# Kernel optimization log

Hardware: AMD Instinct MI355X
Metric: run time of the kernel (lower is better)

## Reference

```python
import jax, jax.numpy as jnp
import numpy as np

N_HEAD = 16
W = 128  # one-sided window = attention_window // 2


def setup_inputs() -> dict:
    key = jax.random.key(0)
    ks = jax.random.split(key, 6)
    B, S, D = 4, 1536, 1024
    init = lambda k: jax.random.normal(k, (D, D), jnp.float32) * 0.02
    return {
        "x": jax.random.normal(ks[0], (B, S, D), jnp.float32),
        "Wq": init(ks[1]), "bq": jnp.zeros((D,), jnp.float32),
        "Wk": init(ks[2]),
        "Wv": init(ks[3]), "bv": jnp.zeros((D,), jnp.float32),
        "Wo": init(ks[4]), "bo": jnp.zeros((D,), jnp.float32),
    }


def _local_attention(q, k, v, w):
    """Sliding-window attention. q,k,v: [B,H,S,Dh]; q,k pre-scaled.
    Returns context [B,H,S,Dh] and banded logits qk [B,S,H,2w+1] (fp32)."""
    B, H, S, Dh = q.shape
    C = S // w  # number of w-sized query chunks
    pad = [(0, 0), (0, 0), (w, w), (0, 0)]
    kp = jnp.pad(k, pad)
    vp = jnp.pad(v, pad)
    # key/value chunks: chunk c sees padded positions [c*w, c*w + 3w)
    idx = jnp.arange(C)[:, None] * w + jnp.arange(3 * w)[None, :]  # [C,3w]
    kc = kp[:, :, idx]                      # [B,H,C,3w,Dh]
    vc = vp[:, :, idx]                      # [B,H,C,3w,Dh]
    qc = q.reshape(B, H, C, w, Dh)          # [B,H,C,w,Dh]
    scores = jnp.einsum('bhcxd,bhcyd->bhcxy', qc, kc)  # [B,H,C,w,3w]
    # extract diagonal band: query x attends to chunk-local keys y = x .. x+2w
    xi = jnp.arange(w)[:, None]             # [w,1]
    jj = jnp.arange(2 * w + 1)[None, :]     # [1,2w+1]
    y = xi + jj                             # [w,2w+1], values in [0,3w)
    band = jnp.take_along_axis(scores, y[None, None, None], axis=-1)  # [B,H,C,w,2w+1]
    # mask positions whose absolute key index falls outside [0,S)
    key_pos = jnp.arange(C)[:, None, None] * w + xi[None] + jj[None] - w  # [C,w,2w+1]
    valid = (key_pos >= 0) & (key_pos < S)
    band = jnp.where(valid[None, None], band, -jnp.inf)
    prob = jax.nn.softmax(band.astype(jnp.float32), axis=-1).astype(q.dtype)
    # scatter band probs back to chunk layout, then contract with value chunks
    scat = jnp.zeros_like(scores).at[..., xi, y].set(prob)  # [B,H,C,w,3w]
    ctx = jnp.einsum('bhcxy,bhcyd->bhcxd', scat, vc).reshape(B, H, S, Dh)
    qk = band.astype(jnp.float32).reshape(B, H, S, 2 * w + 1).transpose(0, 2, 1, 3)
    return ctx, qk


def reference(x, Wq, bq, Wk, Wv, bv, Wo, bo):
    B, S, D = x.shape
    H, Dh = N_HEAD, D // N_HEAD
    scale = Dh ** (-0.25)
    q = ((x @ Wq.T + bq).reshape(B, S, H, Dh).transpose(0, 2, 1, 3)) * scale
    k = ((x @ Wk.T).reshape(B, S, H, Dh).transpose(0, 2, 1, 3)) * scale
    v = (x @ Wv.T + bv).reshape(B, S, H, Dh).transpose(0, 2, 1, 3)
    ctx, qk = _local_attention(q, k, v, W)
    wv = ctx.transpose(0, 2, 1, 3).reshape(B, S, D)
    out = wv @ Wo.T + bo
    return out, qk
```

## Files before the change

### kernel.cpp

```cpp
#include <hip/hip_runtime.h>

#define S_LEN  1536
#define NH     16
#define DHEAD  64
#define WIN    128
#define BAND   257
#define DMODEL 1024
#define BATCH  4
#define MROWS  (BATCH * S_LEN)

#define SQ    32
#define SWIN  (SQ + 2*WIN)
#define WKEYS 320
#define PST   296

#define NEG_BIG (-3.0e38f)

typedef __attribute__((ext_vector_type(8))) short frag_ab;
typedef __attribute__((ext_vector_type(4))) float frag_cd;
typedef __attribute__((ext_vector_type(8))) unsigned short ushort8v;

__device__ __forceinline__ unsigned short f2bf(float f) {
  unsigned u = __float_as_uint(f);
  u += 0x7FFFu + ((u >> 16) & 1u);
  return (unsigned short)(u >> 16);
}
__device__ __forceinline__ float bf2f(unsigned short h) {
  return __uint_as_float(((unsigned)h) << 16);
}

__device__ __forceinline__ void gload16(const unsigned short* g, unsigned short* l) {
  __builtin_amdgcn_global_load_lds(
      (const __attribute__((address_space(1))) unsigned int*)g,
      (__attribute__((address_space(3))) unsigned int*)l, 16, 0, 0);
}

__device__ __forceinline__ int swz4(int r) { return (r & 3) ^ ((r >> 2) & 3); }

__global__ __launch_bounds__(256)
void convert_hilo(const float* __restrict__ src, unsigned short* __restrict__ hi,
                  unsigned short* __restrict__ lo, int n4)
{
  const int i = blockIdx.x * 256 + threadIdx.x;
  if (i >= n4) return;
  const float4 v = reinterpret_cast<const float4*>(src)[i];
  unsigned short h0 = f2bf(v.x), h1 = f2bf(v.y), h2 = f2bf(v.z), h3 = f2bf(v.w);
  unsigned short l0 = f2bf(v.x - bf2f(h0)), l1 = f2bf(v.y - bf2f(h1));
  unsigned short l2 = f2bf(v.z - bf2f(h2)), l3 = f2bf(v.w - bf2f(h3));
  uint2 hp, lp;
  hp.x = (unsigned)h0 | ((unsigned)h1 << 16); hp.y = (unsigned)h2 | ((unsigned)h3 << 16);
  lp.x = (unsigned)l0 | ((unsigned)l1 << 16); lp.y = (unsigned)l2 | ((unsigned)l3 << 16);
  reinterpret_cast<uint2*>(hi)[i] = hp;
  reinterpret_cast<uint2*>(lo)[i] = lp;
}

__global__ __launch_bounds__(256)
void mfma_gemm_qkv(const unsigned short* __restrict__ Ah_g,
                   const unsigned short* __restrict__ Al_g,
                   const unsigned short* __restrict__ Bh_g,
                   const unsigned short* __restrict__ Bl_g,
                   const float* __restrict__ bq, const float* __restrict__ bv,
                   float scale,
                   unsigned short* __restrict__ Qh, unsigned short* __restrict__ Ql,
                   unsigned short* __restrict__ Kh, unsigned short* __restrict__ Kl,
                   unsigned short* __restrict__ Vh, unsigned short* __restrict__ Vl)
{
  __shared__ __align__(16) unsigned short Ah[256*32];
  __shared__ __align__(16) unsigned short Al[256*32];
  __shared__ __align__(16) unsigned short Bh[128*32];
  __shared__ __align__(16) unsigned short Bl[128*32];

  const int t    = threadIdx.x;
  const int wave = t >> 6, lane = t & 63;
  const int wr   = wave >> 1, wc = wave & 1;

  const int bid  = blockIdx.x;
  const int xcd  = bid & 7;
  const int r    = bid >> 3;
  const int n0   = (xcd*3 + (r % 3)) * 128;
  const int m0   = (r / 3) * 256;

  frag_cd acc[8][4];
#pragma unroll
  for (int i = 0; i < 8; ++i)
#pragma unroll
    for (int j = 0; j < 4; ++j) acc[i][j] = (frag_cd){0.f,0.f,0.f,0.f};

  const int srow = lane >> 2;
  const int scol = ((lane & 3) ^ swz4(srow)) * 8;
  const unsigned short* aSh = Ah_g + (size_t)(m0 + wave*64 + srow) * DMODEL + scol;
  const unsigned short* aSl = Al_g + (size_t)(m0 + wave*64 + srow) * DMODEL + scol;
  const unsigned short* bSh = Bh_g + (size_t)(n0 + wave*32 + srow) * DMODEL + scol;
  const unsigned short* bSl = Bl_g + (size_t)(n0 + wave*32 + srow) * DMODEL + scol;
  unsigned short* aDh = &Ah[(wave*64)*32];
  unsigned short* aDl = &Al[(wave*64)*32];
  unsigned short* bDh = &Bh[(wave*32)*32];
  unsigned short* bDl = &Bl[(wave*32)*32];

  const int l16  = lane & 15;
  const int koff = ((lane >> 4) * 8) ^ (swz4(l16) * 8);
  int ofsA[8], ofsB[4];
#pragma unroll
  for (int i = 0; i < 8; ++i) ofsA[i] = (wr*128 + i*16 + l16)*32 + koff;
#pragma unroll
  for (int j = 0; j < 4; ++j) ofsB[j] = (wc*64 + j*16 + l16)*32 + koff;

  for (int k0 = 0; k0 < DMODEL; k0 += 32) {
#pragma unroll
    for (int u = 0; u < 4; ++u) {
      gload16(aSh + (size_t)u*16*DMODEL + k0, aDh + u*16*32);
      gload16(aSl + (size_t)u*16*DMODEL + k0, aDl + u*16*32);
    }
#pragma unroll
    for (int u = 0; u < 2; ++u) {
      gload16(bSh + (size_t)u*16*DMODEL + k0, bDh + u*16*32);
      gload16(bSl + (size_t)u*16*DMODEL + k0, bDl + u*16*32);
    }
    __syncthreads();

    frag_ab bh[4], blr[4];
#pragma unroll
    for (int j = 0; j < 4; ++j) {
      bh[j]  = *reinterpret_cast<const frag_ab*>(&Bh[ofsB[j]]);
      blr[j] = *reinterpret_cast<const frag_ab*>(&Bl[ofsB[j]]);
    }
#pragma unroll
    for (int i = 0; i < 8; ++i) {
      frag_ab ah  = *reinterpret_cast<const frag_ab*>(&Ah[ofsA[i]]);
      frag_ab alr = *reinterpret_cast<const frag_ab*>(&Al[ofsA[i]]);
#pragma unroll
      for (int j = 0; j < 4; ++j) {
        acc[i][j] = __builtin_amdgcn_mfma_f32_16x16x32_bf16(ah,  bh[j],  acc[i][j], 0,0,0);
        acc[i][j] = __builtin_amdgcn_mfma_f32_16x16x32_bf16(ah,  blr[j], acc[i][j], 0,0,0);
        acc[i][j] = __builtin_amdgcn_mfma_f32_16x16x32_bf16(alr, bh[j],  acc[i][j], 0,0,0);
      }
    }
    __syncthreads();
  }

  const int rg = lane >> 4;
  const int which = n0 >> 10;
  const float sc = (which < 2) ? scale : 1.0f;
  const float* bias = (which == 0) ? bq : ((which == 2) ? bv : nullptr);
  unsigned short* Dh = (which == 0) ? Qh : ((which == 1) ? Kh : Vh);
  unsigned short* Dl = (which == 0) ? Ql : ((which == 1) ? Kl : Vl);
#pragma unroll
  for (int j = 0; j < 4; ++j) {
    const int n  = n0 + wc*64 + j*16 + l16;
    const int nn = n & 1023;
    const float bval = bias ? bias[nn] : 0.f;
    const int hh = nn >> 6, dh = nn & 63;
#pragma unroll
    for (int i = 0; i < 8; ++i) {
#pragma unroll
      for (int r2 = 0; r2 < 4; ++r2) {
        const int m = m0 + wr*128 + i*16 + rg*4 + r2;
        const int b = m / S_LEN;
        const int s = m - b * S_LEN;
        const size_t idx = ((size_t)((b*NH + hh)*S_LEN + s))*DHEAD + dh;
        const float v = (acc[i][j][r2] + bval) * sc;
        const unsigned short hv = f2bf(v);
        Dh[idx] = hv;
        Dl[idx] = f2bf(v - bf2f(hv));
      }
    }
  }
}

__global__ __launch_bounds__(256)
void mfma_gemm_wo(const unsigned short* __restrict__ Ah_g,
                  const unsigned short* __restrict__ Al_g,
                  const unsigned short* __restrict__ Bh_g,
                  const unsigned short* __restrict__ Bl_g,
                  const float* __restrict__ bias,
                  float* __restrict__ Cf)
{
  __shared__ __align__(16) unsigned short Ah[128*32];
  __shared__ __align__(16) unsigned short Al[128*32];
  __shared__ __align__(16) unsigned short Bh[64*32];
  __shared__ __align__(16) unsigned short Bl[64*32];

  const int t    = threadIdx.x;
  const int wave = t >> 6, lane = t & 63;
  const int wr   = wave >> 1, wc = wave & 1;
  const int m0   = blockIdx.y * 128;
  const int n0   = blockIdx.x * 64;

  frag_cd acc[4][2];
#pragma unroll
  for (int i = 0; i < 4; ++i)
#pragma unroll
    for (int j = 0; j < 2; ++j) acc[i][j] = (frag_cd){0.f,0.f,0.f,0.f};

  const int srow = lane >> 2;
  const int scol = ((lane & 3) ^ swz4(srow)) * 8;
  size_t rbase[2];
#pragma unroll
  for (int u = 0; u < 2; ++u) {
    const int m = m0 + wave*32 + u*16 + srow;
    const int b = m / S_LEN;
    const int s = m - b * S_LEN;
    rbase[u] = ((size_t)(b*NH))*S_LEN*DHEAD + (size_t)s*DHEAD;
  }
  const unsigned short* pb = Bh_g + (size_t)(n0 + wave*16 + srow) * DMODEL + scol;
  const unsigned short* qb = Bl_g + (size_t)(n0 + wave*16 + srow) * DMODEL + scol;
  unsigned short* lA0 = &Ah[(wave*32)*32];
  unsigned short* lA1 = &Ah[(wave*32+16)*32];
  unsigned short* lL0 = &Al[(wave*32)*32];
  unsigned short* lL1 = &Al[(wave*32+16)*32];
  unsigned short* lB  = &Bh[(wave*16)*32];
  unsigned short* lBl = &Bl[(wave*16)*32];

  const int l16  = lane & 15;
  const int koff = ((lane >> 4) * 8) ^ (swz4(l16) * 8);
  int ofsA[4], ofsB[2];
#pragma unroll
  for (int i = 0; i < 4; ++i) ofsA[i] = (wr*64 + i*16 + l16)*32 + koff;
#pragma unroll
  for (int j = 0; j < 2; ++j) ofsB[j] = (wc*32 + j*16 + l16)*32 + koff;

  for (int k0 = 0; k0 < DMODEL; k0 += 32) {
    const int kk = k0 + scol;
    const size_t aoff = ((size_t)(kk >> 6))*(S_LEN*DHEAD) + (kk & 63);
    gload16(Ah_g + rbase[0] + aoff, lA0);
    gload16(Ah_g + rbase[1] + aoff, lA1);
    gload16(Al_g + rbase[0] + aoff, lL0);
    gload16(Al_g + rbase[1] + aoff, lL1);
    gload16(pb, lB);  gload16(qb, lBl);
    pb += 32; qb += 32;
    __syncthreads();

    frag_ab ah[4], alr[4], bh[2], blr[2];
#pragma unroll
    for (int i = 0; i < 4; ++i) {
      ah[i]  = *reinterpret_cast<const frag_ab*>(&Ah[ofsA[i]]);
      alr[i] = *reinterpret_cast<const frag_ab*>(&Al[ofsA[i]]);
    }
#pragma unroll
    for (int j = 0; j < 2; ++j) {
      bh[j]  = *reinterpret_cast<const frag_ab*>(&Bh[ofsB[j]]);
      blr[j] = *reinterpret_cast<const frag_ab*>(&Bl[ofsB[j]]);
    }
#pragma unroll
    for (int i = 0; i < 4; ++i)
#pragma unroll
      for (int j = 0; j < 2; ++j) {
        acc[i][j] = __builtin_amdgcn_mfma_f32_16x16x32_bf16(ah[i],  bh[j],  acc[i][j], 0,0,0);
        acc[i][j] = __builtin_amdgcn_mfma_f32_16x16x32_bf16(ah[i],  blr[j], acc[i][j], 0,0,0);
        acc[i][j] = __builtin_amdgcn_mfma_f32_16x16x32_bf16(alr[i], bh[j],  acc[i][j], 0,0,0);
      }
    __syncthreads();
  }

  const int rg = lane >> 4;
#pragma unroll
  for (int j = 0; j < 2; ++j) {
    const int n = n0 + wc*32 + j*16 + l16;
    const float bval = bias[n];
#pragma unroll
    for (int i = 0; i < 4; ++i) {
#pragma unroll
      for (int r = 0; r < 4; ++r) {
        const int m = m0 + wr*64 + i*16 + rg*4 + r;
        Cf[(size_t)m * DMODEL + n] = acc[i][j][r] + bval;
      }
    }
  }
}

__global__ __launch_bounds__(256, 3)
void attn_fused(const unsigned short* __restrict__ Qh_g, const unsigned short* __restrict__ Ql_g,
                const unsigned short* __restrict__ Kh_g, const unsigned short* __restrict__ Kl_g,
                const unsigned short* __restrict__ Vh_g, const unsigned short* __restrict__ Vl_g,
                float* __restrict__ qk,
                unsigned short* __restrict__ ctx_hi, unsigned short* __restrict__ ctx_lo)
{
  __shared__ __align__(16) unsigned char arena[48384];
  unsigned short* Khs = (unsigned short*)(arena);
  unsigned short* Kls = (unsigned short*)(arena + 20480);
  unsigned short* Qhs = (unsigned short*)(arena + 40960);
  unsigned short* Qls = (unsigned short*)(arena + 43008);
  unsigned short* Pth = (unsigned short*)(arena);
  unsigned short* Ptl = (unsigned short*)(arena + 18944);
  float*          red = (float*)(arena + 37888);
  unsigned short* Vs  = (unsigned short*)(arena + 38912);

  const int t    = threadIdx.x;
  const int wave = t >> 6, lane = t & 63;

  const int lid  = blockIdx.x;
  const int xcd  = lid & 7;
  const int idx  = lid >> 3;
  const int qblk = xcd*6 + (idx % 6);
  const int hb   = idx / 6;
  const int h    = hb & 15, b = hb >> 4;
  const int qa0  = qblk * SQ;
  const int ws0  = qa0 - WIN;

  const size_t ho = (size_t)(b*NH + h) * S_LEN * DHEAD;
  const unsigned short* Qh = Qh_g + ho;
  const unsigned short* Ql = Ql_g + ho;
  const unsigned short* Kh = Kh_g + ho;
  const unsigned short* Kl = Kl_g + ho;
  const unsigned short* Vh = Vh_g + ho;
  const unsigned short* Vl = Vl_g + ho;

  const int l16  = lane & 15;
  const int grp  = lane >> 4;
  const int koff  = grp * 8;
  const int koffs = koff ^ (swz4(l16) * 8);
  const int srow = lane >> 2;
  const int scol = ((lane & 3) ^ swz4(srow)) * 8;

  frag_cd acc[2][5];
#pragma unroll
  for (int tm = 0; tm < 2; ++tm)
#pragma unroll
    for (int tn = 0; tn < 5; ++tn) acc[tm][tn] = (frag_cd){0.f,0.f,0.f,0.f};

  for (int p = 0; p < 2; ++p) {
    const int d0 = p * 32;
    if (p) __syncthreads();
#pragma unroll
    for (int i = 0; i < 5; ++i) {
      const int r0 = wave*80 + i*16;
      const ptrdiff_t g = (ptrdiff_t)(ws0 + r0 + srow) * DHEAD + d0 + scol;
      gload16(Kh + g, &Khs[r0*32]);
      gload16(Kl + g, &Kls[r0*32]);
    }
    if (wave < 2) {
      const unsigned short* src = wave ? Ql : Qh;
      unsigned short* dst = wave ? Qls : Qhs;
#pragma unroll
      for (int i = 0; i < 2; ++i) {
        const ptrdiff_t g = (ptrdiff_t)(qa0 + i*16 + srow) * DHEAD + d0 + scol;
        gload16(src + g, &dst[i*16*32]);
      }
    }
    __syncthreads();

    frag_ab ah[2], al[2];
#pragma unroll
    for (int tm = 0; tm < 2; ++tm) {
      const int o = (tm*16 + l16)*32 + koffs;
      ah[tm] = *reinterpret_cast<const frag_ab*>(&Qhs[o]);
      al[tm] = *reinterpret_cast<const frag_ab*>(&Qls[o]);
    }
#pragma unroll
    for (int tn = 0; tn < 5; ++tn) {
      const int o = (wave*80 + tn*16 + l16)*32 + koffs;
      frag_ab bh = *reinterpret_cast<const frag_ab*>(&Khs[o]);
      frag_ab bl = *reinterpret_cast<const frag_ab*>(&Kls[o]);
#pragma unroll
      for (int tm = 0; tm < 2; ++tm) {
        acc[tm][tn] = __builtin_amdgcn_mfma_f32_16x16x32_bf16(ah[tm], bh, acc[tm][tn], 0,0,0);
        acc[tm][tn] = __builtin_amdgcn_mfma_f32_16x16x32_bf16(ah[tm], bl, acc[tm][tn], 0,0,0);
        acc[tm][tn] = __builtin_amdgcn_mfma_f32_16x16x32_bf16(al[tm], bh, acc[tm][tn], 0,0,0);
      }
    }
  }

#pragma unroll
  for (int tm = 0; tm < 2; ++tm)
#pragma unroll
    for (int tn = 0; tn < 5; ++tn)
#pragma unroll
      for (int r = 0; r < 4; ++r) {
        const int x  = tm*16 + grp*4 + r;
        const int yw = wave*80 + tn*16 + l16;
        const int j  = yw - x;
        const int kp = ws0 + yw;
        const bool ok = (j >= 0) & (j < BAND) & (kp >= 0) & (kp < S_LEN);
        acc[tm][tn][r] = ok ? acc[tm][tn][r] : NEG_BIG;
      }
#pragma unroll
  for (int tm = 0; tm < 2; ++tm)
#pragma unroll
    for (int r = 0; r < 4; ++r) {
      const int x = tm*16 + grp*4 + r;
      float* qrow = qk + ((size_t)(b*S_LEN + qa0 + x)*NH + h) * BAND;
#pragma unroll
      for (int tn = 0; tn < 5; ++tn) {
        const int yw = wave*80 + tn*16 + l16;
        const int j  = yw - x;
        if (j >= 0 && j < BAND) qrow[j] = acc[tm][tn][r];
      }
    }

  __syncthreads();

  const unsigned short* vsrc = (wave == 3) ? Vl : Vh;
  const int vrow0 = (wave == 3) ? 8 : 0;
  ushort8v RA[5], RB[5];

  auto loadVto = [&](int c, ushort8v* R) {
    const int d0 = c*8;
#pragma unroll
    for (int it = 0; it < 5; ++it) {
      const int y = it*64 + lane;
      ushort8v v = {0,0,0,0,0,0,0,0};
      if (y < SWIN) {
        const int kp = ws0 + y;
        if (kp >= 0 && kp < S_LEN)
          v = *reinterpret_cast<const ushort8v*>(vsrc + (size_t)kp*DHEAD + d0);
      }
      R[it] = v;
    }
  };
  auto writeVfrom = [&](ushort8v* R) {
#pragma unroll
    for (int it = 0; it < 5; ++it) {
      const int y = it*64 + lane;
      if (y < SWIN) {
#pragma unroll
        for (int e = 0; e < 8; ++e) Vs[(vrow0 + e)*PST + y] = R[it][e];
      }
    }
  };

  if (wave >= 2) loadVto(0, RA);
#pragma unroll
  for (int tm = 0; tm < 2; ++tm)
#pragma unroll
    for (int r = 0; r < 4; ++r) {
      float m = acc[tm][0][r];
#pragma unroll
      for (int tn = 1; tn < 5; ++tn) m = fmaxf(m, acc[tm][tn][r]);
      m = fmaxf(m, __shfl_xor(m, 1, 64));
      m = fmaxf(m, __shfl_xor(m, 2, 64));
      m = fmaxf(m, __shfl_xor(m, 4, 64));
      m = fmaxf(m, __shfl_xor(m, 8, 64));
      if (l16 == 0) red[(0*4 + wave)*32 + tm*16 + grp*4 + r] = m;
    }
  {
    const uint4 z = make_uint4(0u,0u,0u,0u);
    uint4* pz = reinterpret_cast<uint4*>(arena);
    for (int i = t; i < 37888/16; i += 256) pz[i] = z;
  }
  if (wave >= 2) writeVfrom(RA);
  __syncthreads();

  if (wave >= 2) loadVto(1, RA);
#pragma unroll
  for (int tm = 0; tm < 2; ++tm)
#pragma unroll
    for (int r = 0; r < 4; ++r) {
      const int x = tm*16 + grp*4 + r;
      float m = red[0*128 + 0*32 + x];
      m = fmaxf(m, red[0*128 + 1*32 + x]);
      m = fmaxf(m, red[0*128 + 2*32 + x]);
      m = fmaxf(m, red[0*128 + 3*32 + x]);
      float s = 0.f;
#pragma unroll
      for (int tn = 0; tn < 5; ++tn) {
        const float e = __expf(acc[tm][tn][r] - m);
        acc[tm][tn][r] = e;
        s += e;
      }
      s += __shfl_xor(s, 1, 64);
      s += __shfl_xor(s, 2, 64);
      s += __shfl_xor(s, 4, 64);
      s += __shfl_xor(s, 8, 64);
      if (l16 == 0) red[(1*4 + wave)*32 + x] = s;
    }
  __syncthreads();

#pragma unroll
  for (int tm = 0; tm < 2; ++tm)
#pragma unroll
    for (int r = 0; r < 4; ++r) {
      const int x = tm*16 + grp*4 + r;
      const float gs = red[128 + 0*32 + x] + red[128 + 1*32 + x]
                     + red[128 + 2*32 + x] + red[128 + 3*32 + x];
      const float inv = 1.f / gs;
#pragma unroll
      for (int tn = 0; tn < 5; ++tn) {
        const int yw = wave*80 + tn*16 + l16;
        const int j  = yw - x;
        if (yw < SWIN && j >= 0 && j < BAND) {
          const float p = acc[tm][tn][r] * inv;
          const unsigned short ph = f2bf(p);
          Pth[x*PST + yw] = ph;
          Ptl[x*PST + yw] = f2bf(p - bf2f(ph));
        }
      }
    }
  __syncthreads();

  frag_ab phf[9];
  if (wave < 2) {
#pragma unroll
    for (int ks = 0; ks < 9; ++ks)
      phf[ks] = *reinterpret_cast<const frag_ab*>(&Pth[(wave*16 + l16)*PST + ks*32 + koff]);
  }

#pragma unroll
  for (int c = 0; c < 8; ++c) {
    frag_cd pacc = (frag_cd){0.f,0.f,0.f,0.f};
    if (wave < 2) {
#pragma unroll
      for (int ks = 0; ks < 9; ++ks) {
        const int kk = ks*32 + koff;
        frag_ab pl = *reinterpret_cast<const frag_ab*>(&Ptl[(wave*16 + l16)*PST + kk]);
        frag_ab vb = *reinterpret_cast<const frag_ab*>(&Vs[l16*PST + kk]);
        pacc = __builtin_amdgcn_mfma_f32_16x16x32_bf16(phf[ks], vb, pacc, 0,0,0);
        pacc = __builtin_amdgcn_mfma_f32_16x16x32_bf16(pl,      vb, pacc, 0,0,0);
      }
    } else {
      if (c < 6) loadVto(c + 2, (c & 1) ? RA : RB);
    }
    __syncthreads();
    if (wave < 2) {
#pragma unroll
      for (int r = 0; r < 4; ++r) pacc[r] += __shfl_xor(pacc[r], 8, 64);
      if (l16 < 8) {
        const int d = c*8 + l16;
#pragma unroll
        for (int r = 0; r < 4; ++r) {
          const int x = wave*16 + grp*4 + r;
          const size_t oidx = ho + (size_t)(qa0 + x)*DHEAD + d;
          const float v = pacc[r];
          const unsigned short hv = f2bf(v);
          ctx_hi[oidx] = hv;
          ctx_lo[oidx] = f2bf(v - bf2f(hv));
        }
      }
    } else {
      if (c < 7) writeVfrom((c & 1) ? RB : RA);
    }
    if (c < 7) __syncthreads();
  }
}

extern "C" void kernel_launch(void* const* d_in, const int* in_sizes, int n_in,
                              void* d_out, int out_size, void* d_ws, size_t ws_size,
                              hipStream_t stream) {
  const float* x  = (const float*)d_in[0];
  const float* Wq = (const float*)d_in[1];
  const float* bq = (const float*)d_in[2];
  const float* Wk = (const float*)d_in[3];
  const float* Wv = (const float*)d_in[4];
  const float* bv = (const float*)d_in[5];
  const float* Wo = (const float*)d_in[6];
  const float* bo = (const float*)d_in[7];

  float* out = (float*)d_out;
  float* qk  = out + (size_t)MROWS * DMODEL;

  const size_t NX = (size_t)MROWS * DMODEL;
  const size_t NW = (size_t)DMODEL * DMODEL;

  unsigned short* xh  = (unsigned short*)qk;
  unsigned short* xl  = xh  + NX;
  unsigned short* whc = xl  + NX;
  unsigned short* wlc = whc + 3*NW;

  unsigned short* Qh = (unsigned short*)d_ws;
  unsigned short* Ql = Qh + NX;
  unsigned short* Kh = Ql + NX;
  unsigned short* Kl = Kh + NX;
  unsigned short* Vh = Kl + NX;
  unsigned short* Vl = Vh + NX;

  unsigned short* ctxh = Qh;
  unsigned short* ctxl = Ql;
  unsigned short* woh  = Kh;
  unsigned short* wol  = Kh + NW;

  const float scale = 0.35355339059327373f;

  dim3 blk(256);
  hipLaunchKernelGGL(convert_hilo, dim3(NX/1024), blk, 0, stream, x,  xh,  xl,  (int)(NX/4));
  hipLaunchKernelGGL(convert_hilo, dim3(NW/1024), blk, 0, stream, Wq, whc,        wlc,        (int)(NW/4));
  hipLaunchKernelGGL(convert_hilo, dim3(NW/1024), blk, 0, stream, Wk, whc + NW,   wlc + NW,   (int)(NW/4));
  hipLaunchKernelGGL(convert_hilo, dim3(NW/1024), blk, 0, stream, Wv, whc + 2*NW, wlc + 2*NW, (int)(NW/4));

  hipLaunchKernelGGL(mfma_gemm_qkv, dim3(576), blk, 0, stream,
                     xh, xl, whc, wlc, bq, bv, scale,
                     Qh, Ql, Kh, Kl, Vh, Vl);

  hipLaunchKernelGGL(attn_fused, dim3((S_LEN/SQ)*NH*BATCH), blk, 0, stream,
                     Qh, Ql, Kh, Kl, Vh, Vl, qk, ctxh, ctxl);

  hipLaunchKernelGGL(convert_hilo, dim3(NW/1024), blk, 0, stream, Wo, woh, wol, (int)(NW/4));

  dim3 gg(DMODEL/64, MROWS/128);
  hipLaunchKernelGGL(mfma_gemm_wo, gg, blk, 0, stream, ctxh, ctxl, woh, wol, bo, out);
}
```

Measured before the change: 550.1 us.

## Double-buffer LDS in QKV and Wo GEMMs and shrink QKV tile to 128x128

Both MFMA GEMMs now use two LDS buffers, issuing the global-to-LDS loads for the next K slice before computing on the current one. This drops one barrier per iteration and lets memory latency overlap with MFMA work. The QKV GEMM tile is halved from 256x128 to 128x128 and the grid doubled to 1152 blocks, which adds parallelism and lowers accumulator register pressure. In exchange, each tile gets less operand reuse, and the doubled LDS footprint may limit occupancy.

```diff
diff --git a/kernel.cpp b/kernel.cpp
--- a/kernel.cpp
+++ b/kernel.cpp
@@ -65,10 +65,10 @@
                    unsigned short* __restrict__ Kh, unsigned short* __restrict__ Kl,
                    unsigned short* __restrict__ Vh, unsigned short* __restrict__ Vl)
 {
-  __shared__ __align__(16) unsigned short Ah[256*32];
-  __shared__ __align__(16) unsigned short Al[256*32];
-  __shared__ __align__(16) unsigned short Bh[128*32];
-  __shared__ __align__(16) unsigned short Bl[128*32];
+  __shared__ __align__(16) unsigned short Ah[2][128*32];
+  __shared__ __align__(16) unsigned short Al[2][128*32];
+  __shared__ __align__(16) unsigned short Bh[2][128*32];
+  __shared__ __align__(16) unsigned short Bl[2][128*32];
 
   const int t    = threadIdx.x;
   const int wave = t >> 6, lane = t & 63;
@@ -78,61 +78,62 @@
   const int xcd  = bid & 7;
   const int r    = bid >> 3;
   const int n0   = (xcd*3 + (r % 3)) * 128;
-  const int m0   = (r / 3) * 256;
-
-  frag_cd acc[8][4];
-#pragma unroll
-  for (int i = 0; i < 8; ++i)
+  const int m0   = (r / 3) * 128;
+
+  frag_cd acc[4][4];
+#pragma unroll
+  for (int i = 0; i < 4; ++i)
 #pragma unroll
     for (int j = 0; j < 4; ++j) acc[i][j] = (frag_cd){0.f,0.f,0.f,0.f};
 
   const int srow = lane >> 2;
   const int scol = ((lane & 3) ^ swz4(srow)) * 8;
-  const unsigned short* aSh = Ah_g + (size_t)(m0 + wave*64 + srow) * DMODEL + scol;
-  const unsigned short* aSl = Al_g + (size_t)(m0 + wave*64 + srow) * DMODEL + scol;
-  const unsigned short* bSh = Bh_g + (size_t)(n0 + wave*32 + srow) * DMODEL + scol;
-  const unsigned short* bSl = Bl_g + (size_t)(n0 + wave*32 + srow) * DMODEL + scol;
-  unsigned short* aDh = &Ah[(wave*64)*32];
-  unsigned short* aDl = &Al[(wave*64)*32];
-  unsigned short* bDh = &Bh[(wave*32)*32];
-  unsigned short* bDl = &Bl[(wave*32)*32];
+  const unsigned short* pa0 = Ah_g + (size_t)(m0 + wave*32      + srow) * DMODEL + scol;
+  const unsigned short* pa1 = Ah_g + (size_t)(m0 + wave*32 + 16 + srow) * DMODEL + scol;
+  const unsigned short* qa0 = Al_g + (size_t)(m0 + wave*32      + srow) * DMODEL + scol;
+  const unsigned short* qa1 = Al_g + (size_t)(m0 + wave*32 + 16 + srow) * DMODEL + scol;
+  const unsigned short* pb0 = Bh_g + (size_t)(n0 + wave*32      + srow) * DMODEL + scol;
+  const unsigned short* pb1 = Bh_g + (size_t)(n0 + wave*32 + 16 + srow) * DMODEL + scol;
+  const unsigned short* qb0 = Bl_g + (size_t)(n0 + wave*32      + srow) * DMODEL + scol;
+  const unsigned short* qb1 = Bl_g + (size_t)(n0 + wave*32 + 16 + srow) * DMODEL + scol;
+  const int dA0 = (wave*32)*32, dA1 = (wave*32+16)*32;
 
   const int l16  = lane & 15;
   const int koff = ((lane >> 4) * 8) ^ (swz4(l16) * 8);
-  int ofsA[8], ofsB[4];
-#pragma unroll
-  for (int i = 0; i < 8; ++i) ofsA[i] = (wr*128 + i*16 + l16)*32 + koff;
+  int ofsA[4], ofsB[4];
+#pragma unroll
+  for (int i = 0; i < 4; ++i) ofsA[i] = (wr*64 + i*16 + l16)*32 + koff;
 #pragma unroll
   for (int j = 0; j < 4; ++j) ofsB[j] = (wc*64 + j*16 + l16)*32 + koff;
 
+  auto STAGE = [&](int buf, int k0) {
+    gload16(pa0 + k0, &Ah[buf][dA0]); gload16(pa1 + k0, &Ah[buf][dA1]);
+    gload16(qa0 + k0, &Al[buf][dA0]); gload16(qa1 + k0, &Al[buf][dA1]);
+    gload16(pb0 + k0, &Bh[buf][dA0]); gload16(pb1 + k0, &Bh[buf][dA1]);
+    gload16(qb0 + k0, &Bl[buf][dA0]); gload16(qb1 + k0, &Bl[buf][dA1]);
+  };
+
+  STAGE(0, 0);
+  __syncthreads();
   for (int k0 = 0; k0 < DMODEL; k0 += 32) {
-#pragma unroll
-    for (int u = 0; u < 4; ++u) {
-      gload16(aSh + (size_t)u*16*DMODEL + k0, aDh + u*16*32);
-      gload16(aSl + (size_t)u*16*DMODEL + k0, aDl + u*16*32);
-    }
-#pragma unroll
-    for (int u = 0; u < 2; ++u) {
-      gload16(bSh + (size_t)u*16*DMODEL + k0, bDh + u*16*32);
-      gload16(bSl + (size_t)u*16*DMODEL + k0, bDl + u*16*32);
-    }
-    __syncthreads();
-
-    frag_ab bh[4], blr[4];
+    const int cur = (k0 >> 5) & 1;
+    if (k0 + 32 < DMODEL) STAGE(cur ^ 1, k0 + 32);
+
+    frag_ab ah[4], alr[4];
+#pragma unroll
+    for (int i = 0; i < 4; ++i) {
+      ah[i]  = *reinterpret_cast<const frag_ab*>(&Ah[cur][ofsA[i]]);
+      alr[i] = *reinterpret_cast<const frag_ab*>(&Al[cur][ofsA[i]]);
+    }
 #pragma unroll
     for (int j = 0; j < 4; ++j) {
-      bh[j]  = *reinterpret_cast<const frag_ab*>(&Bh[ofsB[j]]);
-      blr[j] = *reinterpret_cast<const frag_ab*>(&Bl[ofsB[j]]);
-    }
-#pragma unroll
-    for (int i = 0; i < 8; ++i) {
-      frag_ab ah  = *reinterpret_cast<const frag_ab*>(&Ah[ofsA[i]]);
-      frag_ab alr = *reinterpret_cast<const frag_ab*>(&Al[ofsA[i]]);
-#pragma unroll
-      for (int j = 0; j < 4; ++j) {
-        acc[i][j] = __builtin_amdgcn_mfma_f32_16x16x32_bf16(ah,  bh[j],  acc[i][j], 0,0,0);
-        acc[i][j] = __builtin_amdgcn_mfma_f32_16x16x32_bf16(ah,  blr[j], acc[i][j], 0,0,0);
-        acc[i][j] = __builtin_amdgcn_mfma_f32_16x16x32_bf16(alr, bh[j],  acc[i][j], 0,0,0);
+      frag_ab bh  = *reinterpret_cast<const frag_ab*>(&Bh[cur][ofsB[j]]);
+      frag_ab blr = *reinterpret_cast<const frag_ab*>(&Bl[cur][ofsB[j]]);
+#pragma unroll
+      for (int i = 0; i < 4; ++i) {
+        acc[i][j] = __builtin_amdgcn_mfma_f32_16x16x32_bf16(ah[i],  bh,  acc[i][j], 0,0,0);
+        acc[i][j] = __builtin_amdgcn_mfma_f32_16x16x32_bf16(ah[i],  blr, acc[i][j], 0,0,0);
+        acc[i][j] = __builtin_amdgcn_mfma_f32_16x16x32_bf16(alr[i], bh,  acc[i][j], 0,0,0);
       }
     }
     __syncthreads();
@@ -151,10 +152,10 @@
     const float bval = bias ? bias[nn] : 0.f;
     const int hh = nn >> 6, dh = nn & 63;
 #pragma unroll
-    for (int i = 0; i < 8; ++i) {
+    for (int i = 0; i < 4; ++i) {
 #pragma unroll
       for (int r2 = 0; r2 < 4; ++r2) {
-        const int m = m0 + wr*128 + i*16 + rg*4 + r2;
+        const int m = m0 + wr*64 + i*16 + rg*4 + r2;
         const int b = m / S_LEN;
         const int s = m - b * S_LEN;
         const size_t idx = ((size_t)((b*NH + hh)*S_LEN + s))*DHEAD + dh;
@@ -175,10 +176,10 @@
                   const float* __restrict__ bias,
                   float* __restrict__ Cf)
 {
-  __shared__ __align__(16) unsigned short Ah[128*32];
-  __shared__ __align__(16) unsigned short Al[128*32];
-  __shared__ __align__(16) unsigned short Bh[64*32];
-  __shared__ __align__(16) unsigned short Bl[64*32];
+  __shared__ __align__(16) unsigned short Ah[2][128*32];
+  __shared__ __align__(16) unsigned short Al[2][128*32];
+  __shared__ __align__(16) unsigned short Bh[2][64*32];
+  __shared__ __align__(16) unsigned short Bl[2][64*32];
 
   const int t    = threadIdx.x;
   const int wave = t >> 6, lane = t & 63;
@@ -204,12 +205,8 @@
   }
   const unsigned short* pb = Bh_g + (size_t)(n0 + wave*16 + srow) * DMODEL + scol;
   const unsigned short* qb = Bl_g + (size_t)(n0 + wave*16 + srow) * DMODEL + scol;
-  unsigned short* lA0 = &Ah[(wave*32)*32];
-  unsigned short* lA1 = &Ah[(wave*32+16)*32];
-  unsigned short* lL0 = &Al[(wave*32)*32];
-  unsigned short* lL1 = &Al[(wave*32+16)*32];
-  unsigned short* lB  = &Bh[(wave*16)*32];
-  unsigned short* lBl = &Bl[(wave*16)*32];
+  const int dA0 = (wave*32)*32, dA1 = (wave*32+16)*32;
+  const int dB  = (wave*16)*32;
 
   const int l16  = lane & 15;
   const int koff = ((lane >> 4) * 8) ^ (swz4(l16) * 8);
@@ -219,27 +216,33 @@
 #pragma unroll
   for (int j = 0; j < 2; ++j) ofsB[j] = (wc*32 + j*16 + l16)*32 + koff;
 
-  for (int k0 = 0; k0 < DMODEL; k0 += 32) {
+  auto STAGE = [&](int buf, int k0) {
     const int kk = k0 + scol;
     const size_t aoff = ((size_t)(kk >> 6))*(S_LEN*DHEAD) + (kk & 63);
-    gload16(Ah_g + rbase[0] + aoff, lA0);
-    gload16(Ah_g + rbase[1] + aoff, lA1);
-    gload16(Al_g + rbase[0] + aoff, lL0);
-    gload16(Al_g + rbase[1] + aoff, lL1);
-    gload16(pb, lB);  gload16(qb, lBl);
-    pb += 32; qb += 32;
-    __syncthreads();
+    gload16(Ah_g + rbase[0] + aoff, &Ah[buf][dA0]);
+    gload16(Ah_g + rbase[1] + aoff, &Ah[buf][dA1]);
+    gload16(Al_g + rbase[0] + aoff, &Al[buf][dA0]);
+    gload16(Al_g + rbase[1] + aoff, &Al[buf][dA1]);
+    gload16(pb + k0, &Bh[buf][dB]);
+    gload16(qb + k0, &Bl[buf][dB]);
+  };
+
+  STAGE(0, 0);
+  __syncthreads();
+  for (int k0 = 0; k0 < DMODEL; k0 += 32) {
+    const int cur = (k0 >> 5) & 1;
+    if (k0 + 32 < DMODEL) STAGE(cur ^ 1, k0 + 32);
 
     frag_ab ah[4], alr[4], bh[2], blr[2];
 #pragma unroll
     for (int i = 0; i < 4; ++i) {
-      ah[i]  = *reinterpret_cast<const frag_ab*>(&Ah[ofsA[i]]);
-      alr[i] = *reinterpret_cast<const frag_ab*>(&Al[ofsA[i]]);
+      ah[i]  = *reinterpret_cast<const frag_ab*>(&Ah[cur][ofsA[i]]);
+      alr[i] = *reinterpret_cast<const frag_ab*>(&Al[cur][ofsA[i]]);
     }
 #pragma unroll
     for (int j = 0; j < 2; ++j) {
-      bh[j]  = *reinterpret_cast<const frag_ab*>(&Bh[ofsB[j]]);
-      blr[j] = *reinterpret_cast<const frag_ab*>(&Bl[ofsB[j]]);
+      bh[j]  = *reinterpret_cast<const frag_ab*>(&Bh[cur][ofsB[j]]);
+      blr[j] = *reinterpret_cast<const frag_ab*>(&Bl[cur][ofsB[j]]);
     }
 #pragma unroll
     for (int i = 0; i < 4; ++i)
@@ -575,7 +578,7 @@
   hipLaunchKernelGGL(convert_hilo, dim3(NW/1024), blk, 0, stream, Wk, whc + NW,   wlc + NW,   (int)(NW/4));
   hipLaunchKernelGGL(convert_hilo, dim3(NW/1024), blk, 0, stream, Wv, whc + 2*NW, wlc + 2*NW, (int)(NW/4));
 
-  hipLaunchKernelGGL(mfma_gemm_qkv, dim3(576), blk, 0, stream,
+  hipLaunchKernelGGL(mfma_gemm_qkv, dim3(1152), blk, 0, stream,
                      xh, xl, whc, wlc, bq, bv, scale,
                      Qh, Ql, Kh, Kl, Vh, Vl);
 
```

Result: faster. 470.5 us (-14.5%).
